# Performance work log

Measured on AMD Instinct MI355X. Metric: run time of the kernel, lower is better.

Reference implementation:

```python
import jax, jax.numpy as jnp
import numpy as np

HID = 128
IN = 4

def _lstm_cell(x, h, c, Wih, Whh, bih, bhh):
    # PyTorch LSTMCell: gates ordered i, f, g, o
    gates = x @ Wih.T + bih + h @ Whh.T + bhh  # [B, 4*HID]
    i, f, g, o = jnp.split(gates, 4, axis=-1)
    c_new = jax.nn.sigmoid(f) * c + jax.nn.sigmoid(i) * jnp.tanh(g)
    h_new = jax.nn.sigmoid(o) * jnp.tanh(c_new)
    return h_new, c_new


def setup_inputs() -> dict:
    key = jax.random.key(0)
    ks = jax.random.split(key, 12)
    T, B = 2048, 2048
    s = 1.0 / np.sqrt(HID)  # torch LSTMCell/Linear init scale (1/sqrt(hidden))
    u = lambda k, shape, sc: jax.random.uniform(k, shape, jnp.float32, -sc, sc)
    inp = {
        "input": jax.random.normal(ks[0], (T, B, IN), jnp.float32),
        "future": 0,
        "W_ih1": u(ks[1], (4 * HID, IN), s),
        "W_hh1": u(ks[2], (4 * HID, HID), s),
        "b_ih1": u(ks[3], (4 * HID,), s),
        "b_hh1": u(ks[4], (4 * HID,), s),
        "W_ih2": u(ks[5], (4 * HID, HID), s),
        "W_hh2": u(ks[6], (4 * HID, HID), s),
        "b_ih2": u(ks[7], (4 * HID,), s),
        "b_hh2": u(ks[8], (4 * HID,), s),
        "W_lin": u(ks[9], (IN, HID), s),
        "b_lin": u(ks[10], (IN,), s),
        "h0": jnp.zeros((B, HID), jnp.float32),
        "c0": jnp.zeros((B, HID), jnp.float32),
        "h02": jnp.zeros((B, HID), jnp.float32),
        "c02": jnp.zeros((B, HID), jnp.float32),
    }
    return inp


def reference(input, future, W_ih1, W_hh1, b_ih1, b_hh1, W_ih2, W_hh2, b_ih2, b_hh2,
              W_lin, b_lin, h0, c0, h02, c02):
    # alpha=1 default => teacher forcing on every step (branch never taken), future=0
    def step(carry, x_t):
        h1, c1, h2, c2 = carry
        h1, c1 = _lstm_cell(x_t, h1, c1, W_ih1, W_hh1, b_ih1, b_hh1)
        h2, c2 = _lstm_cell(h1, h2, c2, W_ih2, W_hh2, b_ih2, b_hh2)
        out = h2 @ W_lin.T + b_lin  # [B, 4]
        return (h1, c1, h2, c2), out

    _, outputs = jax.lax.scan(step, (h0, c0, h02, c02), input)
    return outputs  # [T, B, 4]
```

## Files before the change

kernel.cpp:

```cpp
#include <hip/hip_runtime.h>

#define T_STEPS 2048
#define BATCH   2048
#define HIDN    128

typedef short v8s __attribute__((ext_vector_type(8)));
typedef float v4f __attribute__((ext_vector_type(4)));
typedef unsigned short u16;
typedef unsigned int   u32;

#define LDS_W1    0
#define LDS_H1    131072
#define LDS_H2    (131072 + 8192)
#define LDS_TOTAL (131072 + 16384)

__device__ __forceinline__ u16 f2bf(float x) {
    u32 u = __float_as_uint(x);
    u32 r = (u + 0x7FFFu + ((u >> 16) & 1u)) >> 16;
    return (u16)r;
}
__device__ __forceinline__ float rcpf(float x) { return __builtin_amdgcn_rcpf(x); }
__device__ __forceinline__ float sigf(float x) { return rcpf(1.0f + __expf(-x)); }
__device__ __forceinline__ float tanhf_(float x) {
    float e = __expf(2.0f * x);
    return 1.0f - 2.0f * rcpf(e + 1.0f);
}
__device__ __forceinline__ int fragoff(int r, int k) {
    return ((k >> 5) << 10) + ((((k >> 3) & 3) * 16 + r) << 4) + ((k & 7) << 1);
}

__global__ __launch_bounds__(512, 2) void lstm_seq_kernel(
    const float* __restrict__ input,
    const float* __restrict__ W_ih1, const float* __restrict__ W_hh1,
    const float* __restrict__ b_ih1, const float* __restrict__ b_hh1,
    const float* __restrict__ W_ih2, const float* __restrict__ W_hh2,
    const float* __restrict__ b_ih2, const float* __restrict__ b_hh2,
    const float* __restrict__ W_lin, const float* __restrict__ b_lin,
    const float* __restrict__ h0,  const float* __restrict__ c0,
    const float* __restrict__ h02, const float* __restrict__ c02,
    float* __restrict__ out)
{
    extern __shared__ char smem[];
    const int tid = threadIdx.x;
    const int w   = tid >> 6;
    const int l   = tid & 63;
    const int u   = l & 15;
    const int q   = l >> 4;
    const int b0  = blockIdx.x * 8;
    const bool low = (q < 2);
    const int j   = w * 16 + u;

    for (int e = tid; e < 4096; e += 512)
        ((float*)(smem + LDS_H1))[e] = 0.0f;
    __syncthreads();
    for (int e = tid; e < 1024; e += 512) {
        int m = e >> 7, jj = e & 127;
        u16 hv1 = f2bf(h0 [(b0 + m) * HIDN + jj]);
        u16 hv2 = f2bf(h02[(b0 + m) * HIDN + jj]);
        int fo = fragoff(m, jj);
        *(u16*)(smem + LDS_H1 + 4096 + fo)       = hv1;
        *(u16*)(smem + LDS_H1 + 4096 + fo + 128) = hv1;
        *(u16*)(smem + LDS_H2 + 4096 + fo)       = hv2;
    }

    #pragma unroll
    for (int tl = 0; tl < 4; ++tl) {
        int r = tl * 128 + j;
        #pragma unroll
        for (int kt = 0; kt < 4; ++kt) {
            const float* src = W_hh1 + r * HIDN + kt * 32 + q * 8;
            v8s f;
            #pragma unroll
            for (int b = 0; b < 8; ++b) f[b] = (short)f2bf(src[b]);
            *(v8s*)(smem + LDS_W1 + (((w * 4 + tl) * 4 + kt) << 10) + l * 16) = f;
        }
    }

    v8s w2[4][8];
    #pragma unroll
    for (int tl = 0; tl < 4; ++tl) {
        int r = tl * 128 + j;
        #pragma unroll
        for (int kt = 0; kt < 8; ++kt) {
            const float* src = (kt < 4) ? (W_ih2 + r * HIDN + kt * 32 + q * 8)
                                        : (W_hh2 + r * HIDN + (kt - 4) * 32 + q * 8);
            v8s f;
            #pragma unroll
            for (int b = 0; b < 8; ++b) f[b] = (short)f2bf(src[b]);
            w2[tl][kt] = f;
        }
    }
    v8s wx[4];
    #pragma unroll
    for (int tl = 0; tl < 4; ++tl) {
        int r = tl * 128 + j;
        v8s f;
        #pragma unroll
        for (int b = 0; b < 8; ++b) {
            int k = q * 8 + b;
            f[b] = (k < 4) ? (short)f2bf(W_ih1[r * 4 + k]) : (short)0;
        }
        wx[tl] = f;
    }
    v8s wlin[4];
    if (w == 7) {
        #pragma unroll
        for (int kt = 0; kt < 4; ++kt) {
            v8s f;
            #pragma unroll
            for (int b = 0; b < 8; ++b) {
                int kk = kt * 32 + q * 8 + b;
                f[b] = (u < 4) ? (short)f2bf(W_lin[u * HIDN + kk]) : (short)0;
            }
            wlin[kt] = f;
        }
    }

    float bg[4];
    #pragma unroll
    for (int g = 0; g < 4; ++g)
        bg[g] = low ? (b_ih2[g * 128 + j] + b_hh2[g * 128 + j])
                    : (b_ih1[g * 128 + j] + b_hh1[g * 128 + j]);
    float blin = (w == 7 && u < 4) ? b_lin[u] : 0.0f;
    float c[4];
    #pragma unroll
    for (int d = 0; d < 4; ++d) {
        int m = low ? (4 * q + d) : (4 * (q - 2) + d);
        c[d] = low ? c02[(b0 + m) * HIDN + j] : c0[(b0 + m) * HIDN + j];
    }
    float4 xcur = {0, 0, 0, 0}, xnext = {0, 0, 0, 0};
    if (q == 0 && u >= 8)
        xcur = *(const float4*)(input + (long)(b0 + u - 8) * 4);

    const int cb = fragoff(0, j);
    __syncthreads();

    for (int s = 0; s <= T_STEPS; ++s) {
        const char* h1r = smem + LDS_H1 + ((s - 1) & 1) * 4096;
        const char* h2r = smem + LDS_H2 + (s & 1) * 4096;

        v8s a1[4];
        #pragma unroll
        for (int kt = 0; kt < 4; ++kt)
            a1[kt] = *(const v8s*)(h1r + (kt << 10) + l * 16);

        v4f accL2[4], accL1[4];

        if (s >= 1) {
            v8s a2[4];
            #pragma unroll
            for (int kt = 0; kt < 4; ++kt)
                a2[kt] = *(const v8s*)(h2r + (kt << 10) + l * 16);
            #pragma unroll
            for (int tl = 0; tl < 4; ++tl) {
                v4f a = {0.f, 0.f, 0.f, 0.f};
                #pragma unroll
                for (int kt = 0; kt < 4; ++kt)
                    a = __builtin_amdgcn_mfma_f32_16x16x32_bf16(a1[kt], w2[tl][kt], a, 0, 0, 0);
                #pragma unroll
                for (int kt = 0; kt < 4; ++kt)
                    a = __builtin_amdgcn_mfma_f32_16x16x32_bf16(a2[kt], w2[tl][kt + 4], a, 0, 0, 0);
                accL2[tl] = a;
            }
            if (w == 7 && s >= 2) {
                v4f oa = {0.f, 0.f, 0.f, 0.f};
                #pragma unroll
                for (int kt = 0; kt < 4; ++kt)
                    oa = __builtin_amdgcn_mfma_f32_16x16x32_bf16(a2[kt], wlin[kt], oa, 0, 0, 0);
                if (low && u < 4) {
                    #pragma unroll
                    for (int d = 0; d < 4; ++d)
                        out[((long)(s - 2) * BATCH + b0 + 4 * q + d) * 4 + u] = oa[d] + blin;
                }
            }
        }

        if (s < T_STEPS) {
            v8s ax = {0, 0, 0, 0, 0, 0, 0, 0};
            if (q == 0 && u >= 8) {
                ax[0] = (short)f2bf(xcur.x); ax[1] = (short)f2bf(xcur.y);
                ax[2] = (short)f2bf(xcur.z); ax[3] = (short)f2bf(xcur.w);
            }
            if (q == 0 && u >= 8 && s + 1 < T_STEPS)
                xnext = *(const float4*)(input + ((long)(s + 1) * BATCH + b0 + u - 8) * 4);
            #pragma unroll
            for (int tl = 0; tl < 4; ++tl) {
                v4f a = {0.f, 0.f, 0.f, 0.f};
                #pragma unroll
                for (int kt = 0; kt < 4; ++kt) {
                    v8s wf = *(const v8s*)(smem + LDS_W1 + (((w * 4 + tl) * 4 + kt) << 10) + l * 16);
                    a = __builtin_amdgcn_mfma_f32_16x16x32_bf16(a1[kt], wf, a, 0, 0, 0);
                }
                a = __builtin_amdgcn_mfma_f32_16x16x32_bf16(ax, wx[tl], a, 0, 0, 0);
                accL1[tl] = a;
            }
        }

        bool act_en = low ? (s >= 1) : (s < T_STEPS);
        if (act_en) {
            int rbase = low ? (4 * q) : (4 * (q - 2));
            char* hw = (char*)smem + (low ? (LDS_H2 + ((s - 1) & 1) * 4096)
                                          : (LDS_H1 + (s & 1) * 4096));
            #pragma unroll
            for (int d = 0; d < 4; ++d) {
                float gI = (low ? accL2[0][d] : accL1[0][d]) + bg[0];
                float gF = (low ? accL2[1][d] : accL1[1][d]) + bg[1];
                float gG = (low ? accL2[2][d] : accL1[2][d]) + bg[2];
                float gO = (low ? accL2[3][d] : accL1[3][d]) + bg[3];
                float si = sigf(gI), sf = sigf(gF), tg = tanhf_(gG), so = sigf(gO);
                c[d] = sf * c[d] + si * tg;
                float h = so * tanhf_(c[d]);
                u16 hb = f2bf(h);
                int r = rbase + d;
                *(u16*)(hw + cb + (r << 4)) = hb;
                if (!low) *(u16*)(hw + cb + (r << 4) + 128) = hb;
            }
        }
        xcur = xnext;
        __syncthreads();
    }

    if (w == 7) {
        const char* h2r = smem + LDS_H2 + ((T_STEPS - 1) & 1) * 4096;
        v4f oa = {0.f, 0.f, 0.f, 0.f};
        #pragma unroll
        for (int kt = 0; kt < 4; ++kt) {
            v8s a = *(const v8s*)(h2r + (kt << 10) + l * 16);
            oa = __builtin_amdgcn_mfma_f32_16x16x32_bf16(a, wlin[kt], oa, 0, 0, 0);
        }
        if (low && u < 4) {
            #pragma unroll
            for (int d = 0; d < 4; ++d)
                out[((long)(T_STEPS - 1) * BATCH + b0 + 4 * q + d) * 4 + u] = oa[d] + blin;
        }
    }
}

extern "C" void kernel_launch(void* const* d_in, const int* in_sizes, int n_in,
                              void* d_out, int out_size, void* d_ws, size_t ws_size,
                              hipStream_t stream) {
    const float* input = (const float*)d_in[0];
    const float* W_ih1 = (const float*)d_in[2];
    const float* W_hh1 = (const float*)d_in[3];
    const float* b_ih1 = (const float*)d_in[4];
    const float* b_hh1 = (const float*)d_in[5];
    const float* W_ih2 = (const float*)d_in[6];
    const float* W_hh2 = (const float*)d_in[7];
    const float* b_ih2 = (const float*)d_in[8];
    const float* b_hh2 = (const float*)d_in[9];
    const float* W_lin = (const float*)d_in[10];
    const float* b_lin = (const float*)d_in[11];
    const float* h0    = (const float*)d_in[12];
    const float* c0    = (const float*)d_in[13];
    const float* h02   = (const float*)d_in[14];
    const float* c02   = (const float*)d_in[15];
    float* out = (float*)d_out;

    (void)hipFuncSetAttribute((const void*)lstm_seq_kernel,
                              hipFuncAttributeMaxDynamicSharedMemorySize, LDS_TOTAL);
    lstm_seq_kernel<<<BATCH / 8, 512, LDS_TOTAL, stream>>>(
        input, W_ih1, W_hh1, b_ih1, b_hh1, W_ih2, W_hh2, b_ih2, b_hh2,
        W_lin, b_lin, h0, c0, h02, c02, out);
}
```

Before: 3.566 ms.

## Split gate activations across half-waves via lane shuffles, fold biases into MFMA accumulators

```diff
diff --git a/kernel.cpp b/kernel.cpp
--- a/kernel.cpp
+++ b/kernel.cpp
@@ -28,6 +28,8 @@
 __device__ __forceinline__ int fragoff(int r, int k) {
     return ((k >> 5) << 10) + ((((k >> 3) & 3) * 16 + r) << 4) + ((k & 7) << 1);
 }
+
+#define MFMA_BF16 __builtin_amdgcn_mfma_f32_16x16x32_bf16
 
 __global__ __launch_bounds__(512, 2) void lstm_seq_kernel(
     const float* __restrict__ input,
@@ -49,6 +51,7 @@
     const int b0  = blockIdx.x * 8;
     const bool low = (q < 2);
     const int j   = w * 16 + u;
+    const int m0  = ((q & 1) << 2) | ((q >> 1) << 1);
 
     for (int e = tid; e < 4096; e += 512)
         ((float*)(smem + LDS_H1))[e] = 0.0f;
@@ -116,18 +119,20 @@
         }
     }
 
-    float bg[4];
-    #pragma unroll
-    for (int g = 0; g < 4; ++g)
-        bg[g] = low ? (b_ih2[g * 128 + j] + b_hh2[g * 128 + j])
-                    : (b_ih1[g * 128 + j] + b_hh1[g * 128 + j]);
+    float b1g[4], b2g[4];
+    #pragma unroll
+    for (int g = 0; g < 4; ++g) {
+        b1g[g] = b_ih1[g * 128 + j] + b_hh1[g * 128 + j];
+        b2g[g] = b_ih2[g * 128 + j] + b_hh2[g * 128 + j];
+    }
     float blin = (w == 7 && u < 4) ? b_lin[u] : 0.0f;
+
     float c[4];
-    #pragma unroll
-    for (int d = 0; d < 4; ++d) {
-        int m = low ? (4 * q + d) : (4 * (q - 2) + d);
-        c[d] = low ? c02[(b0 + m) * HIDN + j] : c0[(b0 + m) * HIDN + j];
-    }
+    c[0] = c02[(b0 + m0)     * HIDN + j];
+    c[1] = c02[(b0 + m0 + 1) * HIDN + j];
+    c[2] = c0 [(b0 + m0)     * HIDN + j];
+    c[3] = c0 [(b0 + m0 + 1) * HIDN + j];
+
     float4 xcur = {0, 0, 0, 0}, xnext = {0, 0, 0, 0};
     if (q == 0 && u >= 8)
         xcur = *(const float4*)(input + (long)(b0 + u - 8) * 4);
@@ -139,13 +144,15 @@
         const char* h1r = smem + LDS_H1 + ((s - 1) & 1) * 4096;
         const char* h2r = smem + LDS_H2 + (s & 1) * 4096;
 
+        if (q == 0 && u >= 8 && s + 1 < T_STEPS)
+            xnext = *(const float4*)(input + ((long)(s + 1) * BATCH + b0 + u - 8) * 4);
+
         v8s a1[4];
         #pragma unroll
         for (int kt = 0; kt < 4; ++kt)
             a1[kt] = *(const v8s*)(h1r + (kt << 10) + l * 16);
 
-        v4f accL2[4], accL1[4];
-
+        v4f accL2[4];
         if (s >= 1) {
             v8s a2[4];
             #pragma unroll
@@ -153,20 +160,20 @@
                 a2[kt] = *(const v8s*)(h2r + (kt << 10) + l * 16);
             #pragma unroll
             for (int tl = 0; tl < 4; ++tl) {
-                v4f a = {0.f, 0.f, 0.f, 0.f};
+                v4f a = {b2g[tl], b2g[tl], b2g[tl], b2g[tl]};
                 #pragma unroll
                 for (int kt = 0; kt < 4; ++kt)
-                    a = __builtin_amdgcn_mfma_f32_16x16x32_bf16(a1[kt], w2[tl][kt], a, 0, 0, 0);
+                    a = MFMA_BF16(a1[kt], w2[tl][kt], a, 0, 0, 0);
                 #pragma unroll
                 for (int kt = 0; kt < 4; ++kt)
-                    a = __builtin_amdgcn_mfma_f32_16x16x32_bf16(a2[kt], w2[tl][kt + 4], a, 0, 0, 0);
+                    a = MFMA_BF16(a2[kt], w2[tl][kt + 4], a, 0, 0, 0);
                 accL2[tl] = a;
             }
             if (w == 7 && s >= 2) {
                 v4f oa = {0.f, 0.f, 0.f, 0.f};
                 #pragma unroll
                 for (int kt = 0; kt < 4; ++kt)
-                    oa = __builtin_amdgcn_mfma_f32_16x16x32_bf16(a2[kt], wlin[kt], oa, 0, 0, 0);
+                    oa = MFMA_BF16(a2[kt], wlin[kt], oa, 0, 0, 0);
                 if (low && u < 4) {
                     #pragma unroll
                     for (int d = 0; d < 4; ++d)
@@ -175,47 +182,75 @@
             }
         }
 
+        if (s >= 1) {
+            float e0[4], e1[4];
+            #pragma unroll
+            for (int g = 0; g < 4; ++g) {
+                float s2 = __shfl_xor(accL2[g][2], 32, 64);
+                float s3 = __shfl_xor(accL2[g][3], 32, 64);
+                e0[g] = low ? accL2[g][0] : s2;
+                e1[g] = low ? accL2[g][1] : s3;
+            }
+            char* hw = (char*)smem + LDS_H2 + ((s - 1) & 1) * 4096;
+            #pragma unroll
+            for (int e = 0; e < 2; ++e) {
+                float gI = e ? e1[0] : e0[0];
+                float gF = e ? e1[1] : e0[1];
+                float gG = e ? e1[2] : e0[2];
+                float gO = e ? e1[3] : e0[3];
+                float si = sigf(gI), sf = sigf(gF), tg = tanhf_(gG), so = sigf(gO);
+                c[e] = sf * c[e] + si * tg;
+                float h = so * tanhf_(c[e]);
+                *(u16*)(hw + cb + ((m0 + e) << 4)) = f2bf(h);
+            }
+        }
+
+        v4f accL1[4];
         if (s < T_STEPS) {
             v8s ax = {0, 0, 0, 0, 0, 0, 0, 0};
             if (q == 0 && u >= 8) {
                 ax[0] = (short)f2bf(xcur.x); ax[1] = (short)f2bf(xcur.y);
                 ax[2] = (short)f2bf(xcur.z); ax[3] = (short)f2bf(xcur.w);
             }
-            if (q == 0 && u >= 8 && s + 1 < T_STEPS)
-                xnext = *(const float4*)(input + ((long)(s + 1) * BATCH + b0 + u - 8) * 4);
             #pragma unroll
             for (int tl = 0; tl < 4; ++tl) {
-                v4f a = {0.f, 0.f, 0.f, 0.f};
+                v4f a = {b1g[tl], b1g[tl], b1g[tl], b1g[tl]};
                 #pragma unroll
                 for (int kt = 0; kt < 4; ++kt) {
-                    v8s wf = *(const v8s*)(smem + LDS_W1 + (((w * 4 + tl) * 4 + kt) << 10) + l * 16);
-                    a = __builtin_amdgcn_mfma_f32_16x16x32_bf16(a1[kt], wf, a, 0, 0, 0);
+                    v8s wf = *(const v8s*)(smem + LDS_W1 +
+                              (((w * 4 + tl) * 4 + kt) << 10) + l * 16);
+                    a = MFMA_BF16(a1[kt], wf, a, 0, 0, 0);
                 }
-                a = __builtin_amdgcn_mfma_f32_16x16x32_bf16(ax, wx[tl], a, 0, 0, 0);
+                a = MFMA_BF16(ax, wx[tl], a, 0, 0, 0);
                 accL1[tl] = a;
             }
         }
 
-        bool act_en = low ? (s >= 1) : (s < T_STEPS);
-        if (act_en) {
-            int rbase = low ? (4 * q) : (4 * (q - 2));
-            char* hw = (char*)smem + (low ? (LDS_H2 + ((s - 1) & 1) * 4096)
-                                          : (LDS_H1 + (s & 1) * 4096));
-            #pragma unroll
-            for (int d = 0; d < 4; ++d) {
-                float gI = (low ? accL2[0][d] : accL1[0][d]) + bg[0];
-                float gF = (low ? accL2[1][d] : accL1[1][d]) + bg[1];
-                float gG = (low ? accL2[2][d] : accL1[2][d]) + bg[2];
-                float gO = (low ? accL2[3][d] : accL1[3][d]) + bg[3];
+        if (s < T_STEPS) {
+            float e0[4], e1[4];
+            #pragma unroll
+            for (int g = 0; g < 4; ++g) {
+                float s0 = __shfl_xor(accL1[g][0], 32, 64);
+                float s1 = __shfl_xor(accL1[g][1], 32, 64);
+                e0[g] = low ? s0 : accL1[g][2];
+                e1[g] = low ? s1 : accL1[g][3];
+            }
+            char* hw = (char*)smem + LDS_H1 + (s & 1) * 4096;
+            #pragma unroll
+            for (int e = 0; e < 2; ++e) {
+                float gI = e ? e1[0] : e0[0];
+                float gF = e ? e1[1] : e0[1];
+                float gG = e ? e1[2] : e0[2];
+                float gO = e ? e1[3] : e0[3];
                 float si = sigf(gI), sf = sigf(gF), tg = tanhf_(gG), so = sigf(gO);
-                c[d] = sf * c[d] + si * tg;
-                float h = so * tanhf_(c[d]);
+                c[2 + e] = sf * c[2 + e] + si * tg;
+                float h = so * tanhf_(c[2 + e]);
                 u16 hb = f2bf(h);
-                int r = rbase + d;
-                *(u16*)(hw + cb + (r << 4)) = hb;
-                if (!low) *(u16*)(hw + cb + (r << 4) + 128) = hb;
-            }
-        }
+                *(u16*)(hw + cb + ((m0 + e) << 4))       = hb;
+                *(u16*)(hw + cb + ((m0 + e + 8) << 4))   = hb;
+            }
+        }
+
         xcur = xnext;
         __syncthreads();
     }
@@ -226,7 +261,7 @@
         #pragma unroll
         for (int kt = 0; kt < 4; ++kt) {
             v8s a = *(const v8s*)(h2r + (kt << 10) + l * 16);
-            oa = __builtin_amdgcn_mfma_f32_16x16x32_bf16(a, wlin[kt], oa, 0, 0, 0);
+            oa = MFMA_BF16(a, wlin[kt], oa, 0, 0, 0);
         }
         if (low && u < 4) {
             #pragma unroll
```

Measured after the change: 4.212 ms. +18.1%, slower.

## Stream layer-1 recurrent weights from global workspace instead of LDS

Applied to the files above, without the earlier changes.

```diff
diff --git a/kernel.cpp b/kernel.cpp
--- a/kernel.cpp
+++ b/kernel.cpp
@@ -8,11 +8,6 @@
 typedef float v4f __attribute__((ext_vector_type(4)));
 typedef unsigned short u16;
 typedef unsigned int   u32;
-
-#define LDS_W1    0
-#define LDS_H1    131072
-#define LDS_H2    (131072 + 8192)
-#define LDS_TOTAL (131072 + 16384)
 
 __device__ __forceinline__ u16 f2bf(float x) {
     u32 u = __float_as_uint(x);
@@ -29,7 +24,251 @@
     return ((k >> 5) << 10) + ((((k >> 3) & 3) * 16 + r) << 4) + ((k & 7) << 1);
 }
 
-__global__ __launch_bounds__(512, 2) void lstm_seq_kernel(
+#define MFMA_BF16 __builtin_amdgcn_mfma_f32_16x16x32_bf16
+
+#define WS_LDS_H2    8192
+#define WS_LDS_WL    16384
+#define WS_LDS_TOTAL 20480
+#define WS_BYTES     131072
+
+__global__ __launch_bounds__(512, 2) void lstm_seq_kernel_ws(
+    const float* __restrict__ input,
+    const float* __restrict__ W_ih1, const float* __restrict__ W_hh1,
+    const float* __restrict__ b_ih1, const float* __restrict__ b_hh1,
+    const float* __restrict__ W_ih2, const float* __restrict__ W_hh2,
+    const float* __restrict__ b_ih2, const float* __restrict__ b_hh2,
+    const float* __restrict__ W_lin, const float* __restrict__ b_lin,
+    const float* __restrict__ h0,  const float* __restrict__ c0,
+    const float* __restrict__ h02, const float* __restrict__ c02,
+    float* __restrict__ out, char* __restrict__ ws)
+{
+    extern __shared__ char smem[];
+    const int tid = threadIdx.x;
+    const int w   = tid >> 6;
+    const int l   = tid & 63;
+    const int u   = l & 15;
+    const int q   = l >> 4;
+    const int b0  = blockIdx.x * 8;
+    const bool low = (q < 2);
+    const int j   = w * 16 + u;
+
+    for (int e = tid; e < 4096; e += 512)
+        ((float*)smem)[e] = 0.0f;
+    __syncthreads();
+    for (int e = tid; e < 1024; e += 512) {
+        int m = e >> 7, jj = e & 127;
+        u16 hv1 = f2bf(h0 [(b0 + m) * HIDN + jj]);
+        u16 hv2 = f2bf(h02[(b0 + m) * HIDN + jj]);
+        int fo = fragoff(m, jj);
+        *(u16*)(smem + 4096 + fo)       = hv1;
+        *(u16*)(smem + 4096 + fo + 128) = hv1;
+        *(u16*)(smem + WS_LDS_H2 + 4096 + fo) = hv2;
+    }
+
+    #pragma unroll
+    for (int tl = 0; tl < 4; ++tl) {
+        int r = tl * 128 + j;
+        #pragma unroll
+        for (int kt = 0; kt < 4; ++kt) {
+            const float* src = W_hh1 + r * HIDN + kt * 32 + q * 8;
+            v8s f;
+            #pragma unroll
+            for (int b = 0; b < 8; ++b) f[b] = (short)f2bf(src[b]);
+            *(v8s*)(ws + ((((w * 4 + tl) * 4 + kt) << 10) + l * 16)) = f;
+        }
+    }
+
+    v8s w2[4][8];
+    #pragma unroll
+    for (int tl = 0; tl < 4; ++tl) {
+        int r = tl * 128 + j;
+        #pragma unroll
+        for (int kt = 0; kt < 8; ++kt) {
+            const float* src = (kt < 4) ? (W_ih2 + r * HIDN + kt * 32 + q * 8)
+                                        : (W_hh2 + r * HIDN + (kt - 4) * 32 + q * 8);
+            v8s f;
+            #pragma unroll
+            for (int b = 0; b < 8; ++b) f[b] = (short)f2bf(src[b]);
+            w2[tl][kt] = f;
+        }
+    }
+    v8s wx[4];
+    #pragma unroll
+    for (int tl = 0; tl < 4; ++tl) {
+        int r = tl * 128 + j;
+        v8s f;
+        #pragma unroll
+        for (int b = 0; b < 8; ++b) {
+            int k = q * 8 + b;
+            f[b] = (k < 4) ? (short)f2bf(W_ih1[r * 4 + k]) : (short)0;
+        }
+        wx[tl] = f;
+    }
+    if (w == 7) {
+        #pragma unroll
+        for (int kt = 0; kt < 4; ++kt) {
+            v8s f;
+            #pragma unroll
+            for (int b = 0; b < 8; ++b) {
+                int kk = kt * 32 + q * 8 + b;
+                f[b] = (u < 4) ? (short)f2bf(W_lin[u * HIDN + kk]) : (short)0;
+            }
+            *(v8s*)(smem + WS_LDS_WL + (kt << 10) + l * 16) = f;
+        }
+    }
+
+    float b1g[4], b2g[4];
+    #pragma unroll
+    for (int g = 0; g < 4; ++g) {
+        b1g[g] = b_ih1[g * 128 + j] + b_hh1[g * 128 + j];
+        b2g[g] = b_ih2[g * 128 + j] + b_hh2[g * 128 + j];
+    }
+    float blin = (w == 7 && u < 4) ? b_lin[u] : 0.0f;
+    float c[4];
+    #pragma unroll
+    for (int d = 0; d < 4; ++d) {
+        int m = low ? (4 * q + d) : (4 * (q - 2) + d);
+        c[d] = low ? c02[(b0 + m) * HIDN + j] : c0[(b0 + m) * HIDN + j];
+    }
+    float4 xcur = {0, 0, 0, 0}, xnext = {0, 0, 0, 0};
+    if (q == 0 && u >= 8)
+        xcur = *(const float4*)(input + (long)(b0 + u - 8) * 4);
+
+    const int cb = fragoff(0, j);
+    __syncthreads();
+
+    const v8s* __restrict__ w1v = (const v8s*)ws;
+
+    for (int s = 0; s <= T_STEPS; ++s) {
+        const char* h1r = smem + ((s - 1) & 1) * 4096;
+        const char* h2r = smem + WS_LDS_H2 + (s & 1) * 4096;
+
+        if (q == 0 && u >= 8 && s + 1 < T_STEPS)
+            xnext = *(const float4*)(input + ((long)(s + 1) * BATCH + b0 + u - 8) * 4);
+
+        v8s wfA[4], wfB[4];
+        if (s < T_STEPS) {
+            #pragma unroll
+            for (int kt = 0; kt < 4; ++kt)
+                wfA[kt] = w1v[(((w * 4 + 0) * 4 + kt) << 6) + l];
+        }
+
+        v8s a1[4];
+        #pragma unroll
+        for (int kt = 0; kt < 4; ++kt)
+            a1[kt] = *(const v8s*)(h1r + (kt << 10) + l * 16);
+
+        v4f accL2[4];
+        if (s >= 1) {
+            v8s a2[4];
+            #pragma unroll
+            for (int kt = 0; kt < 4; ++kt)
+                a2[kt] = *(const v8s*)(h2r + (kt << 10) + l * 16);
+            #pragma unroll
+            for (int tl = 0; tl < 4; ++tl) {
+                v4f a = {b2g[tl], b2g[tl], b2g[tl], b2g[tl]};
+                #pragma unroll
+                for (int kt = 0; kt < 4; ++kt)
+                    a = MFMA_BF16(a1[kt], w2[tl][kt], a, 0, 0, 0);
+                #pragma unroll
+                for (int kt = 0; kt < 4; ++kt)
+                    a = MFMA_BF16(a2[kt], w2[tl][kt + 4], a, 0, 0, 0);
+                accL2[tl] = a;
+            }
+            if (w == 7 && s >= 2) {
+                v4f oa = {0.f, 0.f, 0.f, 0.f};
+                #pragma unroll
+                for (int kt = 0; kt < 4; ++kt) {
+                    v8s wl = *(const v8s*)(smem + WS_LDS_WL + (kt << 10) + l * 16);
+                    oa = MFMA_BF16(a2[kt], wl, oa, 0, 0, 0);
+                }
+                if (low && u < 4) {
+                    #pragma unroll
+                    for (int d = 0; d < 4; ++d)
+                        out[((long)(s - 2) * BATCH + b0 + 4 * q + d) * 4 + u] = oa[d] + blin;
+                }
+            }
+        }
+
+        v4f accL1[4];
+        if (s < T_STEPS) {
+            v8s ax = {0, 0, 0, 0, 0, 0, 0, 0};
+            if (q == 0 && u >= 8) {
+                ax[0] = (short)f2bf(xcur.x); ax[1] = (short)f2bf(xcur.y);
+                ax[2] = (short)f2bf(xcur.z); ax[3] = (short)f2bf(xcur.w);
+            }
+            #pragma unroll
+            for (int tl = 0; tl < 4; ++tl) {
+                if (tl == 0) {
+                    #pragma unroll
+                    for (int kt = 0; kt < 4; ++kt)
+                        wfB[kt] = w1v[(((w * 4 + 1) * 4 + kt) << 6) + l];
+                } else if (tl == 1) {
+                    #pragma unroll
+                    for (int kt = 0; kt < 4; ++kt)
+                        wfA[kt] = w1v[(((w * 4 + 2) * 4 + kt) << 6) + l];
+                } else if (tl == 2) {
+                    #pragma unroll
+                    for (int kt = 0; kt < 4; ++kt)
+                        wfB[kt] = w1v[(((w * 4 + 3) * 4 + kt) << 6) + l];
+                }
+                v4f a = {b1g[tl], b1g[tl], b1g[tl], b1g[tl]};
+                #pragma unroll
+                for (int kt = 0; kt < 4; ++kt) {
+                    v8s wf = (tl & 1) ? wfB[kt] : wfA[kt];
+                    a = MFMA_BF16(a1[kt], wf, a, 0, 0, 0);
+                }
+                a = MFMA_BF16(ax, wx[tl], a, 0, 0, 0);
+                accL1[tl] = a;
+            }
+        }
+
+        bool act_en = low ? (s >= 1) : (s < T_STEPS);
+        if (act_en) {
+            int rbase = low ? (4 * q) : (4 * (q - 2));
+            char* hw = (char*)smem + (low ? (WS_LDS_H2 + ((s - 1) & 1) * 4096)
+                                          : ((s & 1) * 4096));
+            #pragma unroll
+            for (int d = 0; d < 4; ++d) {
+                float gI = low ? accL2[0][d] : accL1[0][d];
+                float gF = low ? accL2[1][d] : accL1[1][d];
+                float gG = low ? accL2[2][d] : accL1[2][d];
+                float gO = low ? accL2[3][d] : accL1[3][d];
+                float si = sigf(gI), sf = sigf(gF), tg = tanhf_(gG), so = sigf(gO);
+                c[d] = sf * c[d] + si * tg;
+                float h = so * tanhf_(c[d]);
+                u16 hb = f2bf(h);
+                int r = rbase + d;
+                *(u16*)(hw + cb + (r << 4)) = hb;
+                if (!low) *(u16*)(hw + cb + (r << 4) + 128) = hb;
+            }
+        }
+        xcur = xnext;
+        __syncthreads();
+    }
+
+    if (w == 7) {
+        const char* h2r = smem + WS_LDS_H2 + ((T_STEPS - 1) & 1) * 4096;
+        v4f oa = {0.f, 0.f, 0.f, 0.f};
+        #pragma unroll
+        for (int kt = 0; kt < 4; ++kt) {
+            v8s a = *(const v8s*)(h2r + (kt << 10) + l * 16);
+            v8s wl = *(const v8s*)(smem + WS_LDS_WL + (kt << 10) + l * 16);
+            oa = MFMA_BF16(a, wl, oa, 0, 0, 0);
+        }
+        if (low && u < 4) {
+            #pragma unroll
+            for (int d = 0; d < 4; ++d)
+                out[((long)(T_STEPS - 1) * BATCH + b0 + 4 * q + d) * 4 + u] = oa[d] + blin;
+        }
+    }
+}
+
+#define FB_LDS_H1    131072
+#define FB_LDS_H2    (131072 + 8192)
+#define FB_LDS_TOTAL (131072 + 16384)
+
+__global__ __launch_bounds__(512, 2) void lstm_seq_kernel_lds(
     const float* __restrict__ input,
     const float* __restrict__ W_ih1, const float* __restrict__ W_hh1,
     const float* __restrict__ b_ih1, const float* __restrict__ b_hh1,
@@ -51,18 +290,17 @@
     const int j   = w * 16 + u;
 
     for (int e = tid; e < 4096; e += 512)
-        ((float*)(smem + LDS_H1))[e] = 0.0f;
+        ((float*)(smem + FB_LDS_H1))[e] = 0.0f;
     __syncthreads();
     for (int e = tid; e < 1024; e += 512) {
         int m = e >> 7, jj = e & 127;
         u16 hv1 = f2bf(h0 [(b0 + m) * HIDN + jj]);
         u16 hv2 = f2bf(h02[(b0 + m) * HIDN + jj]);
         int fo = fragoff(m, jj);
-        *(u16*)(smem + LDS_H1 + 4096 + fo)       = hv1;
-        *(u16*)(smem + LDS_H1 + 4096 + fo + 128) = hv1;
-        *(u16*)(smem + LDS_H2 + 4096 + fo)       = hv2;
-    }
-
+        *(u16*)(smem + FB_LDS_H1 + 4096 + fo)       = hv1;
+        *(u16*)(smem + FB_LDS_H1 + 4096 + fo + 128) = hv1;
+        *(u16*)(smem + FB_LDS_H2 + 4096 + fo)       = hv2;
+    }
     #pragma unroll
     for (int tl = 0; tl < 4; ++tl) {
         int r = tl * 128 + j;
@@ -72,10 +310,9 @@
             v8s f;
             #pragma unroll
             for (int b = 0; b < 8; ++b) f[b] = (short)f2bf(src[b]);
-            *(v8s*)(smem + LDS_W1 + (((w * 4 + tl) * 4 + kt) << 10) + l * 16) = f;
-        }
-    }
-
+            *(v8s*)(smem + (((w * 4 + tl) * 4 + kt) << 10) + l * 16) = f;
+        }
+    }
     v8s w2[4][8];
     #pragma unroll
     for (int tl = 0; tl < 4; ++tl) {
@@ -115,7 +352,6 @@
             wlin[kt] = f;
         }
     }
-
     float bg[4];
     #pragma unroll
     for (int g = 0; g < 4; ++g)
@@ -131,21 +367,17 @@
     float4 xcur = {0, 0, 0, 0}, xnext = {0, 0, 0, 0};
     if (q == 0 && u >= 8)
         xcur = *(const float4*)(input + (long)(b0 + u - 8) * 4);
-
     const int cb = fragoff(0, j);
     __syncthreads();
 
     for (int s = 0; s <= T_STEPS; ++s) {
-        const char* h1r = smem + LDS_H1 + ((s - 1) & 1) * 4096;
-        const char* h2r = smem + LDS_H2 + (s & 1) * 4096;
-
+        const char* h1r = smem + FB_LDS_H1 + ((s - 1) & 1) * 4096;
+        const char* h2r = smem + FB_LDS_H2 + (s & 1) * 4096;
         v8s a1[4];
         #pragma unroll
         for (int kt = 0; kt < 4; ++kt)
             a1[kt] = *(const v8s*)(h1r + (kt << 10) + l * 16);
-
         v4f accL2[4], accL1[4];
-
         if (s >= 1) {
             v8s a2[4];
             #pragma unroll
@@ -156,17 +388,17 @@
                 v4f a = {0.f, 0.f, 0.f, 0.f};
                 #pragma unroll
                 for (int kt = 0; kt < 4; ++kt)
-                    a = __builtin_amdgcn_mfma_f32_16x16x32_bf16(a1[kt], w2[tl][kt], a, 0, 0, 0);
+                    a = MFMA_BF16(a1[kt], w2[tl][kt], a, 0, 0, 0);
                 #pragma unroll
                 for (int kt = 0; kt < 4; ++kt)
-                    a = __builtin_amdgcn_mfma_f32_16x16x32_bf16(a2[kt], w2[tl][kt + 4], a, 0, 0, 0);
+                    a = MFMA_BF16(a2[kt], w2[tl][kt + 4], a, 0, 0, 0);
                 accL2[tl] = a;
             }
             if (w == 7 && s >= 2) {
                 v4f oa = {0.f, 0.f, 0.f, 0.f};
                 #pragma unroll
                 for (int kt = 0; kt < 4; ++kt)
-                    oa = __builtin_amdgcn_mfma_f32_16x16x32_bf16(a2[kt], wlin[kt], oa, 0, 0, 0);
+                    oa = MFMA_BF16(a2[kt], wlin[kt], oa, 0, 0, 0);
                 if (low && u < 4) {
                     #pragma unroll
                     for (int d = 0; d < 4; ++d)
@@ -174,7 +406,6 @@
                 }
             }
         }
-
         if (s < T_STEPS) {
             v8s ax = {0, 0, 0, 0, 0, 0, 0, 0};
             if (q == 0 && u >= 8) {
@@ -188,19 +419,18 @@
                 v4f a = {0.f, 0.f, 0.f, 0.f};
                 #pragma unroll
                 for (int kt = 0; kt < 4; ++kt) {
-                    v8s wf = *(const v8s*)(smem + LDS_W1 + (((w * 4 + tl) * 4 + kt) << 10) + l * 16);
-                    a = __builtin_amdgcn_mfma_f32_16x16x32_bf16(a1[kt], wf, a, 0, 0, 0);
+                    v8s wf = *(const v8s*)(smem + (((w * 4 + tl) * 4 + kt) << 10) + l * 16);
+                    a = MFMA_BF16(a1[kt], wf, a, 0, 0, 0);
                 }
-                a = __builtin_amdgcn_mfma_f32_16x16x32_bf16(ax, wx[tl], a, 0, 0, 0);
+                a = MFMA_BF16(ax, wx[tl], a, 0, 0, 0);
                 accL1[tl] = a;
             }
         }
-
         bool act_en = low ? (s >= 1) : (s < T_STEPS);
         if (act_en) {
             int rbase = low ? (4 * q) : (4 * (q - 2));
-            char* hw = (char*)smem + (low ? (LDS_H2 + ((s - 1) & 1) * 4096)
-                                          : (LDS_H1 + (s & 1) * 4096));
+            char* hw = (char*)smem + (low ? (FB_LDS_H2 + ((s - 1) & 1) * 4096)
+                                          : (FB_LDS_H1 + (s & 1) * 4096));
             #pragma unroll
             for (int d = 0; d < 4; ++d) {
                 float gI = (low ? accL2[0][d] : accL1[0][d]) + bg[0];
@@ -221,12 +451,12 @@
     }
 
     if (w == 7) {
-        const char* h2r = smem + LDS_H2 + ((T_STEPS - 1) & 1) * 4096;
+        const char* h2r = smem + FB_LDS_H2 + ((T_STEPS - 1) & 1) * 4096;
         v4f oa = {0.f, 0.f, 0.f, 0.f};
         #pragma unroll
         for (int kt = 0; kt < 4; ++kt) {
             v8s a = *(const v8s*)(h2r + (kt << 10) + l * 16);
-            oa = __builtin_amdgcn_mfma_f32_16x16x32_bf16(a, wlin[kt], oa, 0, 0, 0);
+            oa = MFMA_BF16(a, wlin[kt], oa, 0, 0, 0);
         }
         if (low && u < 4) {
             #pragma unroll
@@ -256,9 +486,17 @@
     const float* c02   = (const float*)d_in[15];
     float* out = (float*)d_out;
 
-    (void)hipFuncSetAttribute((const void*)lstm_seq_kernel,
-                              hipFuncAttributeMaxDynamicSharedMemorySize, LDS_TOTAL);
-    lstm_seq_kernel<<<BATCH / 8, 512, LDS_TOTAL, stream>>>(
-        input, W_ih1, W_hh1, b_ih1, b_hh1, W_ih2, W_hh2, b_ih2, b_hh2,
-        W_lin, b_lin, h0, c0, h02, c02, out);
+    if (d_ws != nullptr && ws_size >= WS_BYTES) {
+        (void)hipFuncSetAttribute((const void*)lstm_seq_kernel_ws,
+                                  hipFuncAttributeMaxDynamicSharedMemorySize, WS_LDS_TOTAL);
+        lstm_seq_kernel_ws<<<BATCH / 8, 512, WS_LDS_TOTAL, stream>>>(
+            input, W_ih1, W_hh1, b_ih1, b_hh1, W_ih2, W_hh2, b_ih2, b_hh2,
+            W_lin, b_lin, h0, c0, h02, c02, out, (char*)d_ws);
+    } else {
+        (void)hipFuncSetAttribute((const void*)lstm_seq_kernel_lds,
+                                  hipFuncAttributeMaxDynamicSharedMemorySize, FB_LDS_TOTAL);
+        lstm_seq_kernel_lds<<<BATCH / 8, 512, FB_LDS_TOTAL, stream>>>(
+            input, W_ih1, W_hh1, b_ih1, b_hh1, W_ih2, W_hh2, b_ih2, b_hh2,
+            W_lin, b_lin, h0, c0, h02, c02, out);
+    }
 }
```

Result: slower. 12.77 ms (+258.2%).

## Keep layer-1 recurrent weights in registers instead of LDS and fold biases into accumulators

Applied to the files above, without the earlier changes.

```diff
diff --git a/kernel.cpp b/kernel.cpp
--- a/kernel.cpp
+++ b/kernel.cpp
@@ -9,10 +9,8 @@
 typedef unsigned short u16;
 typedef unsigned int   u32;
 
-#define LDS_W1    0
-#define LDS_H1    131072
-#define LDS_H2    (131072 + 8192)
-#define LDS_TOTAL (131072 + 16384)
+#define LDS_H2    8192
+#define LDS_TOTAL 16384
 
 __device__ __forceinline__ u16 f2bf(float x) {
     u32 u = __float_as_uint(x);
@@ -28,6 +26,8 @@
 __device__ __forceinline__ int fragoff(int r, int k) {
     return ((k >> 5) << 10) + ((((k >> 3) & 3) * 16 + r) << 4) + ((k & 7) << 1);
 }
+
+#define MFMA_BF16 __builtin_amdgcn_mfma_f32_16x16x32_bf16
 
 __global__ __launch_bounds__(512, 2) void lstm_seq_kernel(
     const float* __restrict__ input,
@@ -51,18 +51,19 @@
     const int j   = w * 16 + u;
 
     for (int e = tid; e < 4096; e += 512)
-        ((float*)(smem + LDS_H1))[e] = 0.0f;
+        ((float*)smem)[e] = 0.0f;
     __syncthreads();
     for (int e = tid; e < 1024; e += 512) {
         int m = e >> 7, jj = e & 127;
         u16 hv1 = f2bf(h0 [(b0 + m) * HIDN + jj]);
         u16 hv2 = f2bf(h02[(b0 + m) * HIDN + jj]);
         int fo = fragoff(m, jj);
-        *(u16*)(smem + LDS_H1 + 4096 + fo)       = hv1;
-        *(u16*)(smem + LDS_H1 + 4096 + fo + 128) = hv1;
-        *(u16*)(smem + LDS_H2 + 4096 + fo)       = hv2;
-    }
-
+        *(u16*)(smem + 4096 + fo)       = hv1;
+        *(u16*)(smem + 4096 + fo + 128) = hv1;
+        *(u16*)(smem + LDS_H2 + 4096 + fo) = hv2;
+    }
+
+    v8s w1[4][4];
     #pragma unroll
     for (int tl = 0; tl < 4; ++tl) {
         int r = tl * 128 + j;
@@ -72,10 +73,9 @@
             v8s f;
             #pragma unroll
             for (int b = 0; b < 8; ++b) f[b] = (short)f2bf(src[b]);
-            *(v8s*)(smem + LDS_W1 + (((w * 4 + tl) * 4 + kt) << 10) + l * 16) = f;
-        }
-    }
-
+            w1[tl][kt] = f;
+        }
+    }
     v8s w2[4][8];
     #pragma unroll
     for (int tl = 0; tl < 4; ++tl) {
@@ -116,11 +116,12 @@
         }
     }
 
-    float bg[4];
-    #pragma unroll
-    for (int g = 0; g < 4; ++g)
-        bg[g] = low ? (b_ih2[g * 128 + j] + b_hh2[g * 128 + j])
-                    : (b_ih1[g * 128 + j] + b_hh1[g * 128 + j]);
+    float b1g[4], b2g[4];
+    #pragma unroll
+    for (int g = 0; g < 4; ++g) {
+        b1g[g] = b_ih1[g * 128 + j] + b_hh1[g * 128 + j];
+        b2g[g] = b_ih2[g * 128 + j] + b_hh2[g * 128 + j];
+    }
     float blin = (w == 7 && u < 4) ? b_lin[u] : 0.0f;
     float c[4];
     #pragma unroll
@@ -136,16 +137,18 @@
     __syncthreads();
 
     for (int s = 0; s <= T_STEPS; ++s) {
-        const char* h1r = smem + LDS_H1 + ((s - 1) & 1) * 4096;
+        const char* h1r = smem + ((s - 1) & 1) * 4096;
         const char* h2r = smem + LDS_H2 + (s & 1) * 4096;
+
+        if (q == 0 && u >= 8 && s + 1 < T_STEPS)
+            xnext = *(const float4*)(input + ((long)(s + 1) * BATCH + b0 + u - 8) * 4);
 
         v8s a1[4];
         #pragma unroll
         for (int kt = 0; kt < 4; ++kt)
             a1[kt] = *(const v8s*)(h1r + (kt << 10) + l * 16);
 
-        v4f accL2[4], accL1[4];
-
+        v4f accL2[4];
         if (s >= 1) {
             v8s a2[4];
             #pragma unroll
@@ -153,20 +156,20 @@
                 a2[kt] = *(const v8s*)(h2r + (kt << 10) + l * 16);
             #pragma unroll
             for (int tl = 0; tl < 4; ++tl) {
-                v4f a = {0.f, 0.f, 0.f, 0.f};
-                #pragma unroll
-                for (int kt = 0; kt < 4; ++kt)
-                    a = __builtin_amdgcn_mfma_f32_16x16x32_bf16(a1[kt], w2[tl][kt], a, 0, 0, 0);
-                #pragma unroll
-                for (int kt = 0; kt < 4; ++kt)
-                    a = __builtin_amdgcn_mfma_f32_16x16x32_bf16(a2[kt], w2[tl][kt + 4], a, 0, 0, 0);
+                v4f a = {b2g[tl], b2g[tl], b2g[tl], b2g[tl]};
+                #pragma unroll
+                for (int kt = 0; kt < 4; ++kt)
+                    a = MFMA_BF16(a1[kt], w2[tl][kt], a, 0, 0, 0);
+                #pragma unroll
+                for (int kt = 0; kt < 4; ++kt)
+                    a = MFMA_BF16(a2[kt], w2[tl][kt + 4], a, 0, 0, 0);
                 accL2[tl] = a;
             }
             if (w == 7 && s >= 2) {
                 v4f oa = {0.f, 0.f, 0.f, 0.f};
                 #pragma unroll
                 for (int kt = 0; kt < 4; ++kt)
-                    oa = __builtin_amdgcn_mfma_f32_16x16x32_bf16(a2[kt], wlin[kt], oa, 0, 0, 0);
+                    oa = MFMA_BF16(a2[kt], wlin[kt], oa, 0, 0, 0);
                 if (low && u < 4) {
                     #pragma unroll
                     for (int d = 0; d < 4; ++d)
@@ -175,23 +178,20 @@
             }
         }
 
+        v4f accL1[4];
         if (s < T_STEPS) {
             v8s ax = {0, 0, 0, 0, 0, 0, 0, 0};
             if (q == 0 && u >= 8) {
                 ax[0] = (short)f2bf(xcur.x); ax[1] = (short)f2bf(xcur.y);
                 ax[2] = (short)f2bf(xcur.z); ax[3] = (short)f2bf(xcur.w);
             }
-            if (q == 0 && u >= 8 && s + 1 < T_STEPS)
-                xnext = *(const float4*)(input + ((long)(s + 1) * BATCH + b0 + u - 8) * 4);
             #pragma unroll
             for (int tl = 0; tl < 4; ++tl) {
-                v4f a = {0.f, 0.f, 0.f, 0.f};
-                #pragma unroll
-                for (int kt = 0; kt < 4; ++kt) {
-                    v8s wf = *(const v8s*)(smem + LDS_W1 + (((w * 4 + tl) * 4 + kt) << 10) + l * 16);
-                    a = __builtin_amdgcn_mfma_f32_16x16x32_bf16(a1[kt], wf, a, 0, 0, 0);
-                }
-                a = __builtin_amdgcn_mfma_f32_16x16x32_bf16(ax, wx[tl], a, 0, 0, 0);
+                v4f a = {b1g[tl], b1g[tl], b1g[tl], b1g[tl]};
+                #pragma unroll
+                for (int kt = 0; kt < 4; ++kt)
+                    a = MFMA_BF16(a1[kt], w1[tl][kt], a, 0, 0, 0);
+                a = MFMA_BF16(ax, wx[tl], a, 0, 0, 0);
                 accL1[tl] = a;
             }
         }
@@ -200,13 +200,13 @@
         if (act_en) {
             int rbase = low ? (4 * q) : (4 * (q - 2));
             char* hw = (char*)smem + (low ? (LDS_H2 + ((s - 1) & 1) * 4096)
-                                          : (LDS_H1 + (s & 1) * 4096));
+                                          : ((s & 1) * 4096));
             #pragma unroll
             for (int d = 0; d < 4; ++d) {
-                float gI = (low ? accL2[0][d] : accL1[0][d]) + bg[0];
-                float gF = (low ? accL2[1][d] : accL1[1][d]) + bg[1];
-                float gG = (low ? accL2[2][d] : accL1[2][d]) + bg[2];
-                float gO = (low ? accL2[3][d] : accL1[3][d]) + bg[3];
+                float gI = low ? accL2[0][d] : accL1[0][d];
+                float gF = low ? accL2[1][d] : accL1[1][d];
+                float gG = low ? accL2[2][d] : accL1[2][d];
+                float gO = low ? accL2[3][d] : accL1[3][d];
                 float si = sigf(gI), sf = sigf(gF), tg = tanhf_(gG), so = sigf(gO);
                 c[d] = sf * c[d] + si * tg;
                 float h = so * tanhf_(c[d]);
@@ -226,7 +226,7 @@
         #pragma unroll
         for (int kt = 0; kt < 4; ++kt) {
             v8s a = *(const v8s*)(h2r + (kt << 10) + l * 16);
-            oa = __builtin_amdgcn_mfma_f32_16x16x32_bf16(a, wlin[kt], oa, 0, 0, 0);
+            oa = MFMA_BF16(a, wlin[kt], oa, 0, 0, 0);
         }
         if (low && u < 4) {
             #pragma unroll
```

Result: slower. 12.56 ms (+252.3%).
